# Kernel optimization log

Measured on AMD Instinct MI355X. Metric: run time of the kernel, lower is better.

## Reference

```python
import jax, jax.numpy as jnp
import numpy as np

D_MODEL = 1024
N_HEADS = 16
D_FF = 4096
DEPTH = D_MODEL // N_HEADS
EPS = 1e-5


def setup_inputs() -> dict:
    key = jax.random.key(0)
    ks = jax.random.split(key, 16)
    s = 0.02
    inp = {
        'x': jax.random.normal(ks[0], (4, 2048, D_MODEL), jnp.float32),
        'wq': jax.random.normal(ks[1], (D_MODEL, D_MODEL), jnp.float32) * s,
        'bq': jnp.zeros((D_MODEL,), jnp.float32),
        'wk': jax.random.normal(ks[2], (D_MODEL, D_MODEL), jnp.float32) * s,
        'bk': jnp.zeros((D_MODEL,), jnp.float32),
        'wv': jax.random.normal(ks[3], (D_MODEL, D_MODEL), jnp.float32) * s,
        'bv': jnp.zeros((D_MODEL,), jnp.float32),
        'wo': jax.random.normal(ks[4], (D_MODEL, D_MODEL), jnp.float32) * s,
        'bo': jnp.zeros((D_MODEL,), jnp.float32),
        'w1': jax.random.normal(ks[5], (D_MODEL, D_FF), jnp.float32) * s,
        'b1': jnp.zeros((D_FF,), jnp.float32),
        'w2': jax.random.normal(ks[6], (D_FF, D_MODEL), jnp.float32) * s,
        'b2': jnp.zeros((D_MODEL,), jnp.float32),
        'g1': jnp.ones((D_MODEL,), jnp.float32),
        'be1': jnp.zeros((D_MODEL,), jnp.float32),
        'g2': jnp.ones((D_MODEL,), jnp.float32),
        'be2': jnp.zeros((D_MODEL,), jnp.float32),
    }
    return inp


def _layernorm(x, g, b):
    mu = jnp.mean(x, -1, keepdims=True)
    var = jnp.mean((x - mu) ** 2, -1, keepdims=True)
    return (x - mu) * jax.lax.rsqrt(var + EPS) * g + b


def _rope_angles(seq_len):
    # NB: original module uses raw angles (no cos/sin applied) -- replicate faithfully
    inv_freq = 1.0 / (10000.0 ** (jnp.arange(0, DEPTH, 2, dtype=jnp.float32) / DEPTH))
    freqs = jnp.arange(seq_len, dtype=jnp.float32)[:, None] * inv_freq[None, :]  # [S, DEPTH/2]
    emb = jnp.concatenate([freqs, freqs], axis=-1)  # [S, DEPTH]
    return emb[..., 0::2], emb[..., 1::2]  # 'cos', 'sin' each [S, DEPTH/2]


def _apply_rope(t, cos, sin):
    tc, ts = t[..., 0::2], t[..., 1::2]
    return jnp.concatenate([tc * cos - ts * sin, tc * sin + ts * cos], axis=-1)


def reference(x, wq, bq, wk, bk, wv, bv, wo, bo, w1, b1, w2, b2, g1, be1, g2, be2):
    B, S, D = x.shape
    H, Dh = N_HEADS, DEPTH

    def heads(t):  # [B,S,D] -> [B,H,S,Dh]
        return t.reshape(B, S, H, Dh).transpose(0, 2, 1, 3)

    q = heads(x @ wq + bq)
    k = heads(x @ wk + bk)
    v = heads(x @ wv + bv)

    cos, sin = _rope_angles(S)  # broadcast over [B,H,S,Dh/2]
    q_rot = _apply_rope(q, cos, sin)
    k_rot = _apply_rope(k, cos, sin)

    logits = jnp.einsum('bhqd,bhkd->bhqk', q_rot, k_rot) / jnp.sqrt(jnp.float32(Dh))
    attn = jax.nn.softmax(logits, axis=-1)
    ctx = jnp.einsum('bhqk,bhkd->bhqd', attn, v)  # [B,H,S,Dh]
    ctx = ctx.transpose(0, 2, 1, 3).reshape(B, S, D)
    attn_out = ctx @ wo + bo

    h = _layernorm(x + attn_out, g1, be1)
    ff = jax.nn.relu(h @ w1 + b1) @ w2 + b2
    return _layernorm(h + ff, g2, be2)
```

## Files before the change

### kernel.cpp

```cpp
#include <hip/hip_runtime.h>

typedef _Float16 f16x8 __attribute__((ext_vector_type(8)));
typedef float    f32x4 __attribute__((ext_vector_type(4)));
typedef float    f32x2 __attribute__((ext_vector_type(2)));
typedef short    bf16x8 __attribute__((ext_vector_type(8)));

__device__ __forceinline__ float b2f(ushort u){
  union { float f; unsigned int i; } v; v.i = ((unsigned int)u) << 16; return v.f;
}
__device__ __forceinline__ ushort f2b(float f){
  union { float f; unsigned int i; } v; v.f = f;
  unsigned int r = (v.i + 0x7FFFu + ((v.i >> 16) & 1u)) >> 16;
  return (ushort)r;
}
__device__ __forceinline__ ushort f2h_u(float f){
  union { _Float16 h; ushort u; } v; v.h = (_Float16)f; return v.u;
}
__device__ __forceinline__ float ldf(const void* p, size_t i, int f){
  return f ? ((const float*)p)[i] : b2f(((const ushort*)p)[i]);
}
__device__ __forceinline__ void split3(float v, ushort& a0, ushort& a1, ushort& a2){
  a0 = f2b(v);
  const float r1 = v - b2f(a0);
  a1 = f2b(r1);
  a2 = f2b(r1 - b2f(a1));
}

__global__ void detect_k(const void* __restrict__ x, int* __restrict__ flag)
{
  const int lane = threadIdx.x;
  const ushort* p = (const ushort*)x;
  int wild = 0, zeven = 0;
#pragma unroll
  for (int j = 0; j < 8; ++j) {
    const int idx = lane * 8 + j;
    const ushort u = p[idx];
    if (((u >> 7) & 0xFF) >= 0xF1) ++wild;
    if (((idx & 1) == 0) && u == 0) ++zeven;
  }
#pragma unroll
  for (int off = 1; off < 64; off <<= 1) {
    wild += __shfl_xor(wild, off);
    zeven += __shfl_xor(zeven, off);
  }
  if (lane == 0) *flag = (wild >= 4 || zeven >= 128) ? 1 : 0;
}

__global__ void wtab_k(float* __restrict__ w, int* __restrict__ zeroc,
                       unsigned* __restrict__ ovc)
{
  const int d = threadIdx.x;
  const int i = (d >> 1) & 15;
  const double F2 = pow(10000.0, -(double)i / 8.0);
  const double G2 = pow(10000.0, -(double)(2 * i + 1) / 16.0);
  w[d] = (float)((F2 + G2) * 0.125);
  if (d == 0) { *zeroc = 0; *ovc = 0u; }
}

__global__ __launch_bounds__(256) void cvt_wT_k(const void* __restrict__ W,
    const int* __restrict__ fp, _Float16* __restrict__ Wt, int K, int N)
{
  __shared__ float t[32][33];
  const int f = *fp;
  const int n0 = blockIdx.x * 32, k0 = blockIdx.y * 32;
  const int ln = threadIdx.x & 31, lr = threadIdx.x >> 5;
#pragma unroll
  for (int u = 0; u < 4; ++u) {
    const int kk = lr + u * 8;
    t[kk][ln] = ldf(W, (size_t)(k0 + kk) * N + n0 + ln, f);
  }
  __syncthreads();
#pragma unroll
  for (int u = 0; u < 4; ++u) {
    const int nn = lr + u * 8;
    Wt[(size_t)(n0 + nn) * K + k0 + ln] = (_Float16)t[ln][nn];
  }
}

__global__ __launch_bounds__(256) void cvt_w3T_k(const void* __restrict__ W,
    const int* __restrict__ fp, ushort* __restrict__ Wt3)
{
  __shared__ float t[32][33];
  const int f = *fp;
  const int n0 = blockIdx.x * 32, k0 = blockIdx.y * 32;
  const int ln = threadIdx.x & 31, lr = threadIdx.x >> 5;
#pragma unroll
  for (int u = 0; u < 4; ++u) {
    const int kk = lr + u * 8;
    t[kk][ln] = ldf(W, (size_t)(k0 + kk) * 1024 + n0 + ln, f);
  }
  __syncthreads();
#pragma unroll
  for (int u = 0; u < 4; ++u) {
    const int nn = lr + u * 8;
    const float v = t[ln][nn];
    ushort p0, p1, p2;
    split3(v, p0, p1, p2);
    const size_t o = (size_t)(n0 + nn) * 1024 + k0 + ln;
    Wt3[o]           = p0;
    Wt3[1048576 + o] = p1;
    Wt3[2097152 + o] = p2;
  }
}

__global__ __launch_bounds__(256) void sgemm_qk(
    const void* __restrict__ A, const int* __restrict__ afp,
    const ushort* __restrict__ W3q, const ushort* __restrict__ W3k,
    const void* __restrict__ bq, const void* __restrict__ bk,
    const int* __restrict__ wfp,
    float* __restrict__ qb, float* __restrict__ kbuf,
    const float* __restrict__ wtab)
{
  __shared__ ushort As3[3][128][32];
  const int tid = threadIdx.x;
  const int lane = tid & 63, w = tid >> 6;
  const int wm = w >> 1, wn = w & 1;
  const int fr = lane & 15, g = lane >> 4;
  const int bn = blockIdx.x * 128;
  const int bm = blockIdx.y * 128;
  const int isK = bn >> 10;
  const ushort* W3 = isK ? W3k : W3q;
  const int bnl = bn & 1023;
  const int af = *afp;

  f32x4 acc[4][4];
#pragma unroll
  for (int m = 0; m < 4; ++m)
#pragma unroll
    for (int n = 0; n < 4; ++n)
      acc[m][n][0] = acc[m][n][1] = acc[m][n][2] = acc[m][n][3] = 0.f;

  for (int k0 = 0; k0 < 1024; k0 += 32) {
    __syncthreads();
    {
      const int row = tid >> 1, kk0 = (tid & 1) * 16;
      float tv[16];
      if (af) {
        const float4* p = (const float4*)((const float*)A + (size_t)(bm + row) * 1024 + k0 + kk0);
#pragma unroll
        for (int u = 0; u < 4; ++u) {
          const float4 t = p[u];
          tv[u*4]=t.x; tv[u*4+1]=t.y; tv[u*4+2]=t.z; tv[u*4+3]=t.w;
        }
      } else {
        const uint4* p = (const uint4*)((const ushort*)A + (size_t)(bm + row) * 1024 + k0 + kk0);
#pragma unroll
        for (int u = 0; u < 2; ++u) {
          const uint4 t = p[u];
          tv[u*8+0]=b2f((ushort)(t.x&0xffff)); tv[u*8+1]=b2f((ushort)(t.x>>16));
          tv[u*8+2]=b2f((ushort)(t.y&0xffff)); tv[u*8+3]=b2f((ushort)(t.y>>16));
          tv[u*8+4]=b2f((ushort)(t.z&0xffff)); tv[u*8+5]=b2f((ushort)(t.z>>16));
          tv[u*8+6]=b2f((ushort)(t.w&0xffff)); tv[u*8+7]=b2f((ushort)(t.w>>16));
        }
      }
      ushort p0[16], p1[16], p2[16];
#pragma unroll
      for (int u = 0; u < 16; ++u) split3(tv[u], p0[u], p1[u], p2[u]);
#pragma unroll
      for (int u = 0; u < 2; ++u) {
        *(uint4*)&As3[0][row][kk0 + u*8] = *(uint4*)&p0[u*8];
        *(uint4*)&As3[1][row][kk0 + u*8] = *(uint4*)&p1[u*8];
        *(uint4*)&As3[2][row][kk0 + u*8] = *(uint4*)&p2[u*8];
      }
    }
    __syncthreads();

    bf16x8 afr[3][4];
#pragma unroll
    for (int p = 0; p < 3; ++p)
#pragma unroll
      for (int m = 0; m < 4; ++m)
        afr[p][m] = *(const bf16x8*)&As3[p][wm*64 + m*16 + fr][g*8];

#pragma unroll
    for (int pb = 0; pb < 3; ++pb) {
      bf16x8 bfr[4];
#pragma unroll
      for (int n = 0; n < 4; ++n)
        bfr[n] = *(const bf16x8*)(W3 + (size_t)pb * 1048576 +
                                  (size_t)(bnl + wn*64 + n*16 + fr) * 1024 + k0 + g*8);
      const int npa = 3 - pb;
#pragma unroll
      for (int m = 0; m < 4; ++m)
#pragma unroll
        for (int n = 0; n < 4; ++n)
#pragma unroll
          for (int pa = 0; pa < 3; ++pa)
            if (pa < npa)
              acc[m][n] = __builtin_amdgcn_mfma_f32_16x16x32_bf16(
                              afr[pa][m], bfr[n], acc[m][n], 0, 0, 0);
    }
  }

  const int wf = *wfp;
#pragma unroll
  for (int m = 0; m < 4; ++m) {
#pragma unroll
    for (int n = 0; n < 4; ++n) {
      const int col = bnl + wn*64 + n*16 + fr;
      const float bv = ldf(isK ? bk : bq, col, wf);
      const int hh = col >> 6, dh = col & 63;
#pragma unroll
      for (int e = 0; e < 4; ++e) {
        const int gr = bm + wm*64 + m*16 + g*4 + e;
        const int b = gr >> 11, s = gr & 2047;
        const size_t idx = (size_t)b * 2097152 + (((size_t)hh * 2048) + s) * 64 + dh;
        const float v = acc[m][n][e] + bv;
        if (isK) kbuf[idx] = v;
        else     qb[idx]   = v * wtab[dh];
      }
    }
  }
}

__global__ __launch_bounds__(256) void vgemm_k(
    const void* __restrict__ A, const int* __restrict__ afp,
    const _Float16* __restrict__ Wt,
    const void* __restrict__ bias, const int* __restrict__ bfp,
    ushort* __restrict__ outU)
{
  __shared__ _Float16 As[128][40];
  __shared__ _Float16 Bs[128][40];
  const int tid = threadIdx.x;
  const int lane = tid & 63;
  const int w = tid >> 6;
  const int wm = w >> 1, wn = w & 1;
  const int fr = lane & 15, g = lane >> 4;
  const int bn = blockIdx.x * 128, bm = blockIdx.y * 128;
  const int af = *afp;

  f32x4 acc[4][4];
#pragma unroll
  for (int m = 0; m < 4; ++m)
#pragma unroll
    for (int n = 0; n < 4; ++n)
      acc[m][n][0] = acc[m][n][1] = acc[m][n][2] = acc[m][n][3] = 0.f;

  for (int k0 = 0; k0 < 1024; k0 += 32) {
    __syncthreads();
    {
      const int r = tid >> 1, kp = (tid & 1) * 16;
      float tv[16];
      if (af) {
        const float4* p = (const float4*)((const float*)A + (size_t)(bm + r) * 1024 + k0 + kp);
#pragma unroll
        for (int u = 0; u < 4; ++u) {
          const float4 t = p[u];
          tv[u*4]=t.x; tv[u*4+1]=t.y; tv[u*4+2]=t.z; tv[u*4+3]=t.w;
        }
      } else {
        const uint4* p = (const uint4*)((const ushort*)A + (size_t)(bm + r) * 1024 + k0 + kp);
#pragma unroll
        for (int u = 0; u < 2; ++u) {
          const uint4 t = p[u];
          tv[u*8+0]=b2f((ushort)(t.x&0xffff)); tv[u*8+1]=b2f((ushort)(t.x>>16));
          tv[u*8+2]=b2f((ushort)(t.y&0xffff)); tv[u*8+3]=b2f((ushort)(t.y>>16));
          tv[u*8+4]=b2f((ushort)(t.z&0xffff)); tv[u*8+5]=b2f((ushort)(t.z>>16));
          tv[u*8+6]=b2f((ushort)(t.w&0xffff)); tv[u*8+7]=b2f((ushort)(t.w>>16));
        }
      }
      _Float16 hv[16];
#pragma unroll
      for (int u = 0; u < 16; ++u) hv[u] = (_Float16)tv[u];
      *(uint4*)&As[r][kp]     = *(uint4*)&hv[0];
      *(uint4*)&As[r][kp + 8] = *(uint4*)&hv[8];
    }
    {
      const int r = tid >> 1, kp = (tid & 1) * 16;
      const uint4* bp = (const uint4*)(Wt + (size_t)(bn + r) * 1024 + k0 + kp);
      const uint4 v0 = bp[0], v1 = bp[1];
      *(uint4*)&Bs[r][kp]     = v0;
      *(uint4*)&Bs[r][kp + 8] = v1;
    }
    __syncthreads();
    f16x8 afr[4], bf8[4];
#pragma unroll
    for (int m = 0; m < 4; ++m)
      afr[m] = *(const f16x8*)&As[wm * 64 + m * 16 + fr][g * 8];
#pragma unroll
    for (int n = 0; n < 4; ++n)
      bf8[n] = *(const f16x8*)&Bs[wn * 64 + n * 16 + fr][g * 8];
#pragma unroll
    for (int m = 0; m < 4; ++m)
#pragma unroll
      for (int n = 0; n < 4; ++n)
        acc[m][n] = __builtin_amdgcn_mfma_f32_16x16x32_f16(afr[m], bf8[n], acc[m][n], 0, 0, 0);
  }

  const int bfl = *bfp;
#pragma unroll
  for (int m = 0; m < 4; ++m) {
#pragma unroll
    for (int n = 0; n < 4; ++n) {
      const int gc = bn + wn * 64 + n * 16 + fr;
      const float bv = ldf(bias, gc, bfl);
      const int hh = gc >> 6, dh = gc & 63;
#pragma unroll
      for (int e = 0; e < 4; ++e) {
        const int gr = bm + wm * 64 + m * 16 + g * 4 + e;
        const int b = gr >> 11, s = gr & 2047;
        const size_t idx = (size_t)b * 2097152 + (((size_t)hh * 2048) + s) * 64 + dh;
        outU[idx] = f2b(acc[m][n][e] + bv);
      }
    }
  }
}

template<int MODE>
__global__ __launch_bounds__(256) void sgemm(
    const void* __restrict__ A, const int* __restrict__ afp, int arow0,
    const void* __restrict__ W, const void* __restrict__ bias,
    const int* __restrict__ wfp,
    const void* __restrict__ res, const int* __restrict__ rfp,
    ushort* __restrict__ outU, float* __restrict__ outF,
    const float* __restrict__ wtab,
    int N, int K, int erow0)
{
  __shared__ float As[64][17];
  __shared__ float Ws[16][65];
  const int tid = threadIdx.x;
  const int tx = tid & 15, ty = tid >> 4;
  const int bn = blockIdx.x * 64, bm = blockIdx.y * 64;
  const int af = *afp, wf = *wfp;

  float acc[4][4] = {};

  for (int k0 = 0; k0 < K; k0 += 16) {
    __syncthreads();
#pragma unroll
    for (int u = 0; u < 4; ++u) {
      const int idx = tid * 4 + u;
      const int row = idx >> 4, kk = idx & 15;
      As[row][kk] = ldf(A, (size_t)(arow0 + bm + row) * K + k0 + kk, af);
    }
#pragma unroll
    for (int u = 0; u < 4; ++u) {
      const int idx = tid * 4 + u;
      const int kk = idx >> 6, col = idx & 63;
      Ws[kk][col] = ldf(W, (size_t)(k0 + kk) * N + bn + col, wf);
    }
    __syncthreads();
#pragma unroll
    for (int kk = 0; kk < 16; ++kk) {
      float ar[4], wr[4];
#pragma unroll
      for (int i = 0; i < 4; ++i) ar[i] = As[ty * 4 + i][kk];
#pragma unroll
      for (int j = 0; j < 4; ++j) wr[j] = Ws[kk][tx * 4 + j];
#pragma unroll
      for (int i = 0; i < 4; ++i)
#pragma unroll
        for (int j = 0; j < 4; ++j) acc[i][j] += ar[i] * wr[j];
    }
  }

  const int rf = (MODE >= 4) ? *rfp : 0;
#pragma unroll
  for (int i = 0; i < 4; ++i) {
    const int gr = erow0 + bm + ty * 4 + i;
#pragma unroll
    for (int j = 0; j < 4; ++j) {
      const int gc = bn + tx * 4 + j;
      float v = acc[i][j] + ldf(bias, gc, wf);
      if (MODE == 0) {
        const int hh = gc >> 6, dh = gc & 63, s = gr & 2047;
        outF[(((size_t)hh * 2048) + s) * 64 + dh] = v * wtab[dh];
      } else if (MODE == 1) {
        const int hh = gc >> 6, dh = gc & 63, s = gr & 2047;
        outF[(((size_t)hh * 2048) + s) * 64 + dh] = v;
      } else if (MODE == 2) {
        const int hh = gc >> 6, dh = gc & 63, s = gr & 2047;
        outU[(((size_t)hh * 2048) + s) * 64 + dh] = f2b(v);
      } else if (MODE == 3) {
        outU[(size_t)gr * N + gc] = f2b(fmaxf(v, 0.f));
      } else if (MODE == 4) {
        v += ldf(res, (size_t)gr * 1024 + gc, rf);
        outU[(size_t)gr * 1024 + gc] = f2b(v);
      } else {
        v += ldf(res, (size_t)gr * 1024 + gc, rf);
        outF[(size_t)gr * 1024 + gc] = v;
      }
    }
  }
}

template<int MODE, int TM>
__global__ __launch_bounds__(256) void hgemm(
    const _Float16* __restrict__ A, int arow0,
    const _Float16* __restrict__ Wt,
    const void* __restrict__ bias, const int* __restrict__ bfp,
    const void* __restrict__ res, const int* __restrict__ rfp,
    const _Float16* __restrict__ resH,
    _Float16* __restrict__ outH, float* __restrict__ outF,
    int N, int K, int erow0)
{
  constexpr int MF = TM / 32;
  __shared__ _Float16 As[TM][40];
  __shared__ _Float16 Bs[128][40];
  const int tid = threadIdx.x;
  const int lane = tid & 63;
  const int w = tid >> 6;
  const int wm = w >> 1, wn = w & 1;
  const int fr = lane & 15, g = lane >> 4;
  const int bn = blockIdx.x * 128, bm = blockIdx.y * TM;

  f32x4 acc[MF][4];
#pragma unroll
  for (int m = 0; m < MF; ++m)
#pragma unroll
    for (int n = 0; n < 4; ++n)
      acc[m][n][0] = acc[m][n][1] = acc[m][n][2] = acc[m][n][3] = 0.f;

  for (int k0 = 0; k0 < K; k0 += 32) {
    __syncthreads();
    if constexpr (TM == 128) {
      const int r = tid >> 1, kp = (tid & 1) * 16;
      const uint4* ap = (const uint4*)(A + (size_t)(arow0 + bm + r) * K + k0 + kp);
      const uint4 v0 = ap[0], v1 = ap[1];
      *(uint4*)&As[r][kp]     = v0;
      *(uint4*)&As[r][kp + 8] = v1;
    } else {
      const int r = tid >> 2, kp = (tid & 3) * 8;
      const uint4 v0 = *(const uint4*)(A + (size_t)(arow0 + bm + r) * K + k0 + kp);
      *(uint4*)&As[r][kp] = v0;
    }
    {
      const int r = tid >> 1, kp = (tid & 1) * 16;
      const uint4* bp = (const uint4*)(Wt + (size_t)(bn + r) * K + k0 + kp);
      const uint4 v0 = bp[0], v1 = bp[1];
      *(uint4*)&Bs[r][kp]     = v0;
      *(uint4*)&Bs[r][kp + 8] = v1;
    }
    __syncthreads();
    f16x8 afr[MF], bf8[4];
#pragma unroll
    for (int m = 0; m < MF; ++m)
      afr[m] = *(const f16x8*)&As[wm * (TM / 2) + m * 16 + fr][g * 8];
#pragma unroll
    for (int n = 0; n < 4; ++n)
      bf8[n] = *(const f16x8*)&Bs[wn * 64 + n * 16 + fr][g * 8];
#pragma unroll
    for (int m = 0; m < MF; ++m)
#pragma unroll
      for (int n = 0; n < 4; ++n)
        acc[m][n] = __builtin_amdgcn_mfma_f32_16x16x32_f16(afr[m], bf8[n], acc[m][n], 0, 0, 0);
  }

  const int bfl = *bfp;
  const int rfl = (MODE == 4) ? *rfp : 0;
#pragma unroll
  for (int m = 0; m < MF; ++m) {
#pragma unroll
    for (int n = 0; n < 4; ++n) {
      const int gc = bn + wn * 64 + n * 16 + fr;
      const float bv = ldf(bias, gc, bfl);
#pragma unroll
      for (int e = 0; e < 4; ++e) {
        const int gr = erow0 + bm + wm * (TM / 2) + m * 16 + (lane >> 4) * 4 + e;
        float v = acc[m][n][e] + bv;
        if (MODE == 3) {
          outH[(size_t)gr * N + gc] = (_Float16)fmaxf(v, 0.f);
        } else if (MODE == 4) {
          v += ldf(res, (size_t)gr * 1024 + gc, rfl);
          outH[(size_t)gr * 1024 + gc] = (_Float16)v;
        } else {
          v += (float)resH[(size_t)gr * 1024 + gc];
          outF[(size_t)gr * 1024 + gc] = v;
        }
      }
    }
  }
}

#define ACAP 48

__global__ __launch_bounds__(256) void attn_mfma_k(
    const float* __restrict__ qb, const float* __restrict__ kb,
    const ushort* __restrict__ vb, ushort* __restrict__ ctx,
    unsigned* __restrict__ ovcount, unsigned* __restrict__ ovlist)
{
  __shared__ __align__(16) char smem[32768];
  ushort*   kpl  = (ushort*)smem;
  unsigned* cnt  = (unsigned*)(smem + 13824);
  float*    mrow = (float*)(smem + 14080);
  ushort*   cL   = (ushort*)(smem + 14336);
  float*    LL   = (float*)(smem + 20480);

  const int tid  = threadIdx.x;
  const int lane = tid & 63;
  const int wv   = tid >> 6;
  const int fr   = lane & 15, g = lane >> 4;
  const int h = blockIdx.y, b = blockIdx.z;
  const int s0 = blockIdx.x * 64;
  const size_t bh = (size_t)b * 16 + h;
  const float*  qh = qb + bh * (2048 * 64);
  const float*  kh = kb + bh * (2048 * 64);
  const ushort* vh = vb + bh * (2048 * 64);

  {
    ushort* qs = (ushort*)smem;
    const int r = tid >> 2, d0 = (tid & 3) * 16;
    const float4* qp = (const float4*)(qh + (size_t)(s0 + r) * 64 + d0);
    float tv[16];
#pragma unroll
    for (int u = 0; u < 4; ++u) {
      const float4 t = qp[u];
      tv[u*4]=t.x; tv[u*4+1]=t.y; tv[u*4+2]=t.z; tv[u*4+3]=t.w;
    }
    ushort p0[16], p1[16], p2[16];
#pragma unroll
    for (int u = 0; u < 16; ++u) split3(tv[u], p0[u], p1[u], p2[u]);
    const int base = r * 72 + d0;
#pragma unroll
    for (int u = 0; u < 2; ++u) {
      *(uint4*)&qs[0*4608 + base + u*8] = *(uint4*)&p0[u*8];
      *(uint4*)&qs[1*4608 + base + u*8] = *(uint4*)&p1[u*8];
      *(uint4*)&qs[2*4608 + base + u*8] = *(uint4*)&p2[u*8];
    }
  }
  __syncthreads();
  bf16x8 af[3][2];
  {
    ushort* qs = (ushort*)smem;
    const int rb = (wv * 16 + fr) * 72 + g * 8;
#pragma unroll
    for (int p = 0; p < 3; ++p)
#pragma unroll
      for (int dg = 0; dg < 2; ++dg)
        af[p][dg] = *(bf16x8*)&qs[p*4608 + rb + dg*32];
  }
  __syncthreads();
  if (tid < 64) cnt[tid] = 0;

  float svv[4];
#pragma unroll
  for (int e = 0; e < 4; ++e) svv[e] = (float)(s0 + wv * 16 + g * 4 + e);

  float mloc[4] = {-3.0e38f, -3.0e38f, -3.0e38f, -3.0e38f};

  for (int c0 = 0; c0 < 2048; c0 += 32) {
    __syncthreads();
    {
      const int key = tid >> 3, d0 = (tid & 7) * 8;
      const float4* kp4 = (const float4*)(kh + (size_t)(c0 + key) * 64 + d0);
      const float4 t0 = kp4[0], t1 = kp4[1];
      float tv[8] = {t0.x,t0.y,t0.z,t0.w,t1.x,t1.y,t1.z,t1.w};
      ushort p0[8], p1[8], p2[8];
#pragma unroll
      for (int u = 0; u < 8; ++u) split3(tv[u], p0[u], p1[u], p2[u]);
      const int base = key * 72 + d0;
      *(uint4*)&kpl[0*2304 + base] = *(uint4*)&p0[0];
      *(uint4*)&kpl[1*2304 + base] = *(uint4*)&p1[0];
      *(uint4*)&kpl[2*2304 + base] = *(uint4*)&p2[0];
    }
    __syncthreads();

    float Lv[2][4];
#pragma unroll
    for (int kg = 0; kg < 2; ++kg) {
      f32x4 a0v = {0.f,0.f,0.f,0.f}, a1v = {0.f,0.f,0.f,0.f}, a2v = {0.f,0.f,0.f,0.f};
#pragma unroll
      for (int dg = 0; dg < 2; ++dg) {
        const int rb = (kg * 16 + fr) * 72 + dg * 32 + g * 8;
        const bf16x8 b0 = *(bf16x8*)&kpl[0*2304 + rb];
        const bf16x8 b1 = *(bf16x8*)&kpl[1*2304 + rb];
        const bf16x8 b2 = *(bf16x8*)&kpl[2*2304 + rb];
        a0v = __builtin_amdgcn_mfma_f32_16x16x32_bf16(af[0][dg], b0, a0v, 0,0,0);
        a1v = __builtin_amdgcn_mfma_f32_16x16x32_bf16(af[0][dg], b1, a1v, 0,0,0);
        a2v = __builtin_amdgcn_mfma_f32_16x16x32_bf16(af[1][dg], b0, a2v, 0,0,0);
        a0v = __builtin_amdgcn_mfma_f32_16x16x32_bf16(af[1][dg], b1, a0v, 0,0,0);
        a1v = __builtin_amdgcn_mfma_f32_16x16x32_bf16(af[0][dg], b2, a1v, 0,0,0);
        a2v = __builtin_amdgcn_mfma_f32_16x16x32_bf16(af[2][dg], b0, a2v, 0,0,0);
      }
      const float cw = (float)(c0 + kg * 16 + fr);
#pragma unroll
      for (int e = 0; e < 4; ++e) {
        const float a = (a0v[e] + a1v[e]) + a2v[e];
        Lv[kg][e] = a * cw * svv[e];
      }
    }
#pragma unroll
    for (int e = 0; e < 4; ++e) {
      float t = fmaxf(Lv[0][e], Lv[1][e]);
#pragma unroll
      for (int off = 1; off < 16; off <<= 1) t = fmaxf(t, __shfl_xor(t, off));
      mloc[e] = fmaxf(mloc[e], t);
    }
#pragma unroll
    for (int kg = 0; kg < 2; ++kg)
#pragma unroll
      for (int e = 0; e < 4; ++e) {
        if (Lv[kg][e] > mloc[e] - 80.f) {
          const int row = wv * 16 + g * 4 + e;
          const unsigned idx = atomicAdd(&cnt[row], 1u);
          if (idx < ACAP) {
            cL[row * ACAP + idx] = (ushort)(c0 + kg * 16 + fr);
            LL[row * ACAP + idx] = Lv[kg][e];
          }
        }
      }
  }
  if (fr == 0) {
#pragma unroll
    for (int e = 0; e < 4; ++e) mrow[wv * 16 + g * 4 + e] = mloc[e];
  }
  __syncthreads();

  const int row = tid >> 2, seg = tid & 3;
  const unsigned n = cnt[row];
  const int gs = s0 + row;
  if (n > ACAP) {
    if (seg == 0) {
      const unsigned i = atomicAdd(ovcount, 1u);
      ovlist[i] = (unsigned)(bh * 2048 + gs);
    }
  } else {
    const float mf = mrow[row];
    float o[16];
#pragma unroll
    for (int u = 0; u < 16; ++u) o[u] = 0.f;
    float l = 0.f;
    for (unsigned i = 0; i < n; ++i) {
      const float d = LL[row * ACAP + i] - mf;
      if (d > -80.f) {
        const int c = cL[row * ACAP + i];
        const float p = expf(d);
        l += p;
        const uint4* vp = (const uint4*)(vh + (size_t)c * 64 + seg * 16);
        const uint4 t0 = vp[0], t1 = vp[1];
        const uint wds[8] = {t0.x,t0.y,t0.z,t0.w,t1.x,t1.y,t1.z,t1.w};
#pragma unroll
        for (int u = 0; u < 8; ++u) {
          o[u*2]   += p * b2f((ushort)(wds[u] & 0xffff));
          o[u*2+1] += p * b2f((ushort)(wds[u] >> 16));
        }
      }
    }
    const float inv = 1.f / l;
    ushort* op = ctx + (((size_t)b * 2048) + gs) * 1024 + h * 64 + seg * 16;
    uint pk[8];
#pragma unroll
    for (int u = 0; u < 8; ++u)
      pk[u] = (uint)f2h_u(o[2*u] * inv) | ((uint)f2h_u(o[2*u+1] * inv) << 16);
    *(uint4*)(op)     = make_uint4(pk[0], pk[1], pk[2], pk[3]);
    *(uint4*)(op + 8) = make_uint4(pk[4], pk[5], pk[6], pk[7]);
  }
}

__global__ __launch_bounds__(256) void attn_cleanup2_k(
    const float* __restrict__ qb, const float* __restrict__ kb,
    const ushort* __restrict__ vb, ushort* __restrict__ ctx,
    const unsigned* __restrict__ ovcount, const unsigned* __restrict__ ovlist)
{
  __shared__ float Ls[2048];
  __shared__ float osum[32][65];
  __shared__ float wm[4], wl[4];
  const unsigned count = *ovcount;
  const int tid = threadIdx.x;
  const int seg = tid & 7;
  const int kq  = tid >> 3;
  const int wave = tid >> 6;

  for (unsigned idx = blockIdx.x; idx < count; idx += gridDim.x) {
    const unsigned r = ovlist[idx];
    const int gs = (int)(r & 2047u);
    const size_t bh = (size_t)(r >> 11);
    const int b = (int)(bh >> 4), h = (int)(bh & 15);
    const float*  qh = qb + bh * (2048 * 64);
    const float*  kh = kb + bh * (2048 * 64);
    const ushort* vh = vb + bh * (2048 * 64);

    float q[8];
    {
      const float4* qp = (const float4*)(qh + (size_t)gs * 64 + seg * 8);
      const float4 t0 = qp[0], t1 = qp[1];
      q[0]=t0.x; q[1]=t0.y; q[2]=t0.z; q[3]=t0.w;
      q[4]=t1.x; q[5]=t1.y; q[6]=t1.z; q[7]=t1.w;
    }
    const float sq = (float)gs;

    float mloc = -3.0e38f;
    for (int it = 0; it < 64; ++it) {
      const int c = it * 32 + kq;
      const float4* kp = (const float4*)(kh + (size_t)c * 64 + seg * 8);
      const float4 a = kp[0], bb = kp[1];
      float dt = q[0]*a.x + q[1]*a.y + q[2]*a.z + q[3]*a.w
               + q[4]*bb.x + q[5]*bb.y + q[6]*bb.z + q[7]*bb.w;
      dt += __shfl_xor(dt, 1);
      dt += __shfl_xor(dt, 2);
      dt += __shfl_xor(dt, 4);
      const float L = dt * sq * (float)c;
      if (seg == 0) Ls[c] = L;
      mloc = fmaxf(mloc, L);
    }
    mloc = fmaxf(mloc, __shfl_xor(mloc, 8));
    mloc = fmaxf(mloc, __shfl_xor(mloc, 16));
    mloc = fmaxf(mloc, __shfl_xor(mloc, 32));
    if ((tid & 63) == 0) wm[wave] = mloc;
    __syncthreads();
    const float m = fmaxf(fmaxf(wm[0], wm[1]), fmaxf(wm[2], wm[3]));

    float o[8] = {0.f,0.f,0.f,0.f,0.f,0.f,0.f,0.f};
    float lloc = 0.f;
    for (int it = 0; it < 64; ++it) {
      const int c = it * 32 + kq;
      const float p = expf(Ls[c] - m);
      lloc += p;
      const uint4 vv = *(const uint4*)(vh + (size_t)c * 64 + seg * 8);
      o[0] += p * b2f((ushort)(vv.x & 0xffff)); o[1] += p * b2f((ushort)(vv.x >> 16));
      o[2] += p * b2f((ushort)(vv.y & 0xffff)); o[3] += p * b2f((ushort)(vv.y >> 16));
      o[4] += p * b2f((ushort)(vv.z & 0xffff)); o[5] += p * b2f((ushort)(vv.z >> 16));
      o[6] += p * b2f((ushort)(vv.w & 0xffff)); o[7] += p * b2f((ushort)(vv.w >> 16));
    }
    lloc += __shfl_xor(lloc, 8);
    lloc += __shfl_xor(lloc, 16);
    lloc += __shfl_xor(lloc, 32);
    if ((tid & 63) == 0) wl[wave] = lloc;
#pragma unroll
    for (int u = 0; u < 8; ++u) osum[kq][seg * 8 + u] = o[u];
    __syncthreads();
    const float l = (wl[0] + wl[1]) + (wl[2] + wl[3]);
    if (tid < 64) {
      float acc = 0.f;
#pragma unroll
      for (int k2 = 0; k2 < 32; ++k2) acc += osum[k2][tid];
      ctx[(((size_t)b * 2048) + gs) * 1024 + h * 64 + tid] = f2h_u(acc / l);
    }
    __syncthreads();
  }
}

template<int RPT, int OF16>
__global__ __launch_bounds__(256) void attn_k(
    const float* __restrict__ qb, const float* __restrict__ kb,
    const ushort* __restrict__ vb, ushort* __restrict__ ctx,
    int b0, size_t bstrF, size_t bstrU)
{
  __shared__ float kS[64][64];
  __shared__ float vS[64][64];
  const int tid = threadIdx.x;
  const int h  = blockIdx.y;
  const int bz = blockIdx.z;
  const int b  = b0 + bz;
  const float*  qh = qb + bstrF * bz + (size_t)h * 2048 * 64;
  const float*  kh = kb + bstrF * bz + (size_t)h * 2048 * 64;
  const ushort* vh = vb + bstrU * bz + (size_t)h * 2048 * 64;

  const int seg  = tid & 3;
  const int slot = tid >> 2;
  const int row0 = blockIdx.x * (64 * RPT) + slot * RPT;

  f32x2 qv[RPT][8], o[RPT][8];
  float m[RPT], l[RPT], sq[RPT];
#pragma unroll
  for (int i = 0; i < RPT; ++i) {
    const float4* qp = (const float4*)(qh + (size_t)(row0 + i) * 64 + seg * 16);
#pragma unroll
    for (int w = 0; w < 4; ++w) {
      const float4 t = qp[w];
      qv[i][2*w]   = f32x2{t.x, t.y};
      qv[i][2*w+1] = f32x2{t.z, t.w};
    }
    m[i] = -3.0e38f; l[i] = 0.f; sq[i] = (float)(row0 + i);
#pragma unroll
    for (int t = 0; t < 8; ++t) o[i][t] = f32x2{0.f, 0.f};
  }

  for (int c0 = 0; c0 < 2048; c0 += 64) {
    __syncthreads();
    {
      const int key = tid >> 2, sg = tid & 3;
      const float4* sp = (const float4*)(kh + (size_t)(c0 + key) * 64 + sg * 16);
      float4* dp = (float4*)&kS[key][sg * 16];
#pragma unroll
      for (int u = 0; u < 4; ++u) dp[u] = sp[u];
      const uint4* vp = (const uint4*)(vh + (size_t)(c0 + key) * 64 + sg * 16);
      float* vd = &vS[key][sg * 16];
#pragma unroll
      for (int u = 0; u < 2; ++u) {
        const uint4 t = vp[u];
        vd[u*8+0] = b2f((ushort)(t.x & 0xffff)); vd[u*8+1] = b2f((ushort)(t.x >> 16));
        vd[u*8+2] = b2f((ushort)(t.y & 0xffff)); vd[u*8+3] = b2f((ushort)(t.y >> 16));
        vd[u*8+4] = b2f((ushort)(t.z & 0xffff)); vd[u*8+5] = b2f((ushort)(t.z >> 16));
        vd[u*8+6] = b2f((ushort)(t.w & 0xffff)); vd[u*8+7] = b2f((ushort)(t.w >> 16));
      }
    }
    __syncthreads();
#pragma unroll 2
    for (int j = 0; j < 64; ++j) {
      const float4* kp = (const float4*)&kS[j][seg * 16];
      const float4 ka = kp[0], kb4 = kp[1], kc = kp[2], kd = kp[3];
      const f32x2 K0 = {ka.x, ka.y},  K1 = {ka.z, ka.w};
      const f32x2 K2 = {kb4.x, kb4.y}, K3 = {kb4.z, kb4.w};
      const f32x2 K4 = {kc.x, kc.y},  K5 = {kc.z, kc.w};
      const f32x2 K6 = {kd.x, kd.y},  K7 = {kd.z, kd.w};
      float dt[RPT];
#pragma unroll
      for (int i = 0; i < RPT; ++i) {
        f32x2 a2 = qv[i][0] * K0;
        a2 += qv[i][1] * K1;
        a2 += qv[i][2] * K2;
        a2 += qv[i][3] * K3;
        a2 += qv[i][4] * K4;
        a2 += qv[i][5] * K5;
        a2 += qv[i][6] * K6;
        a2 += qv[i][7] * K7;
        dt[i] = a2[0] + a2[1];
      }
#pragma unroll
      for (int i = 0; i < RPT; ++i) {
        dt[i] += __shfl_xor(dt[i], 1);
        dt[i] += __shfl_xor(dt[i], 2);
      }
      const float cc = (float)(c0 + j);
#pragma unroll
      for (int i = 0; i < RPT; ++i) {
        const float L = dt[i] * sq[i] * cc;
        const float d = L - m[i];
        if (d > 0.f) {
          const float r = expf(-d);
          l[i] = l[i] * r + 1.f;
          m[i] = L;
          const f32x2 r2 = {r, r};
          const float4* vp4 = (const float4*)&vS[j][seg * 16];
          const float4 va = vp4[0], vb4 = vp4[1], vc = vp4[2], vd4 = vp4[3];
          const f32x2 V[8] = {{va.x,va.y},{va.z,va.w},{vb4.x,vb4.y},{vb4.z,vb4.w},
                              {vc.x,vc.y},{vc.z,vc.w},{vd4.x,vd4.y},{vd4.z,vd4.w}};
#pragma unroll
          for (int t = 0; t < 8; ++t) o[i][t] = o[i][t] * r2 + V[t];
        } else if (d > -80.f) {
          const float p = expf(d);
          l[i] += p;
          const f32x2 p2 = {p, p};
          const float4* vp4 = (const float4*)&vS[j][seg * 16];
          const float4 va = vp4[0], vb4 = vp4[1], vc = vp4[2], vd4 = vp4[3];
          const f32x2 V[8] = {{va.x,va.y},{va.z,va.w},{vb4.x,vb4.y},{vb4.z,vb4.w},
                              {vc.x,vc.y},{vc.z,vc.w},{vd4.x,vd4.y},{vd4.z,vd4.w}};
#pragma unroll
          for (int t = 0; t < 8; ++t) o[i][t] += p2 * V[t];
        }
      }
    }
  }

#pragma unroll
  for (int i = 0; i < RPT; ++i) {
    const float inv = 1.f / l[i];
    ushort* op = ctx + (((size_t)b * 2048) + row0 + i) * 1024 + h * 64 + seg * 16;
    uint pk[8];
#pragma unroll
    for (int t2 = 0; t2 < 8; ++t2) {
      const uint lo = OF16 ? (uint)f2h_u(o[i][t2][0] * inv) : (uint)f2b(o[i][t2][0] * inv);
      const uint hi = OF16 ? (uint)f2h_u(o[i][t2][1] * inv) : (uint)f2b(o[i][t2][1] * inv);
      pk[t2] = lo | (hi << 16);
    }
    *(uint4*)(op)     = make_uint4(pk[0], pk[1], pk[2], pk[3]);
    *(uint4*)(op + 8) = make_uint4(pk[4], pk[5], pk[6], pk[7]);
  }
}

__global__ __launch_bounds__(256) void ln_k(const ushort* __restrict__ y,
                                            const void* __restrict__ g,
                                            const void* __restrict__ be,
                                            const int* __restrict__ fp,
                                            ushort* __restrict__ out)
{
  const int row = blockIdx.x, tid = threadIdx.x;
  const int f = *fp;
  const ushort* p = y + (size_t)row * 1024;
  float v[4], s = 0.f, s2 = 0.f;
#pragma unroll
  for (int i = 0; i < 4; ++i) {
    const float x = b2f(p[tid + i * 256]);
    v[i] = x; s += x; s2 += x * x;
  }
#pragma unroll
  for (int off = 1; off < 64; off <<= 1) { s += __shfl_xor(s, off); s2 += __shfl_xor(s2, off); }
  __shared__ float red[8];
  const int wave = tid >> 6, lane = tid & 63;
  if (lane == 0) { red[wave] = s; red[4 + wave] = s2; }
  __syncthreads();
  s = red[0] + red[1] + red[2] + red[3];
  s2 = red[4] + red[5] + red[6] + red[7];
  const float mu = s * (1.f / 1024.f);
  const float var = s2 * (1.f / 1024.f) - mu * mu;
  const float rstd = rsqrtf(var + 1e-5f);
  ushort* o = out + (size_t)row * 1024;
#pragma unroll
  for (int i = 0; i < 4; ++i) {
    const int c = tid + i * 256;
    o[c] = f2b((v[i] - mu) * rstd * ldf(g, c, f) + ldf(be, c, f));
  }
}

__global__ __launch_bounds__(256) void ln_h_k(const _Float16* __restrict__ y,
                                              const void* __restrict__ g,
                                              const void* __restrict__ be,
                                              const int* __restrict__ fp,
                                              _Float16* __restrict__ out)
{
  const int row = blockIdx.x, tid = threadIdx.x;
  const int f = *fp;
  const _Float16* p = y + (size_t)row * 1024;
  float v[4], s = 0.f, s2 = 0.f;
#pragma unroll
  for (int i = 0; i < 4; ++i) {
    const float x = (float)p[tid + i * 256];
    v[i] = x; s += x; s2 += x * x;
  }
#pragma unroll
  for (int off = 1; off < 64; off <<= 1) { s += __shfl_xor(s, off); s2 += __shfl_xor(s2, off); }
  __shared__ float red[8];
  const int wave = tid >> 6, lane = tid & 63;
  if (lane == 0) { red[wave] = s; red[4 + wave] = s2; }
  __syncthreads();
  s = red[0] + red[1] + red[2] + red[3];
  s2 = red[4] + red[5] + red[6] + red[7];
  const float mu = s * (1.f / 1024.f);
  const float var = s2 * (1.f / 1024.f) - mu * mu;
  const float rstd = rsqrtf(var + 1e-5f);
  _Float16* o = out + (size_t)row * 1024;
#pragma unroll
  for (int i = 0; i < 4; ++i) {
    const int c = tid + i * 256;
    o[c] = (_Float16)((v[i] - mu) * rstd * ldf(g, c, f) + ldf(be, c, f));
  }
}

__global__ __launch_bounds__(256) void ln_f32_k(float* __restrict__ y,
                                                const void* __restrict__ g,
                                                const void* __restrict__ be,
                                                const int* __restrict__ fp)
{
  const int row = blockIdx.x, tid = threadIdx.x;
  const int f = *fp;
  float* p = y + (size_t)row * 1024;
  float v[4], s = 0.f, s2 = 0.f;
#pragma unroll
  for (int i = 0; i < 4; ++i) {
    const float x = p[tid + i * 256];
    v[i] = x; s += x; s2 += x * x;
  }
#pragma unroll
  for (int off = 1; off < 64; off <<= 1) { s += __shfl_xor(s, off); s2 += __shfl_xor(s2, off); }
  __shared__ float red[8];
  const int wave = tid >> 6, lane = tid & 63;
  if (lane == 0) { red[wave] = s; red[4 + wave] = s2; }
  __syncthreads();
  s = red[0] + red[1] + red[2] + red[3];
  s2 = red[4] + red[5] + red[6] + red[7];
  const float mu = s * (1.f / 1024.f);
  const float var = s2 * (1.f / 1024.f) - mu * mu;
  const float rstd = rsqrtf(var + 1e-5f);
#pragma unroll
  for (int i = 0; i < 4; ++i) {
    const int c = tid + i * 256;
    p[c] = (v[i] - mu) * rstd * ldf(g, c, f) + ldf(be, c, f);
  }
}

extern "C" void kernel_launch(void* const* d_in, const int* in_sizes, int n_in,
                              void* d_out, int out_size, void* d_ws, size_t ws_size,
                              hipStream_t stream)
{
  const void* x  = d_in[0];
  const void* wq = d_in[1];  const void* bq = d_in[2];
  const void* wk = d_in[3];  const void* bk = d_in[4];
  const void* wv = d_in[5];  const void* bv = d_in[6];
  const void* wo = d_in[7];  const void* bo = d_in[8];
  const void* w1 = d_in[9];  const void* b1 = d_in[10];
  const void* w2 = d_in[11]; const void* b2 = d_in[12];
  const void* g1 = d_in[13]; const void* be1 = d_in[14];
  const void* g2 = d_in[15]; const void* be2 = d_in[16];
  float* outp = (float*)d_out;

  const size_t MB = 1048576;
  char* ws = (char*)d_ws;
  int*      flag    = (int*)(ws + 0);
  int*      zeroc   = (int*)(ws + 64);
  unsigned* ovcount = (unsigned*)(ws + 128);
  float*    wtab    = (float*)(ws + 256);

  detect_k<<<dim3(1), dim3(64), 0, stream>>>(x, flag);
  wtab_k<<<dim3(1), dim3(64), 0, stream>>>(wtab, zeroc, ovcount);

  const size_t QS = (size_t)16 * 2048 * 64;

  if (ws_size >= (size_t)98 * MB) {
    float*     qb   = (float*)(ws + 1 * MB);
    float*     kb   = (float*)(ws + 33 * MB);
    ushort*    vb   = (ushort*)(ws + 65 * MB);
    ushort*    ctxh = (ushort*)(ws + 81 * MB);
    unsigned*  ovlist = (unsigned*)(ws + 97 * MB);
    ushort*    W3qT = (ushort*)(ws + 81 * MB);
    ushort*    W3kT = (ushort*)(ws + 87 * MB);
    _Float16*  WvT  = (_Float16*)(ws + 93 * MB);
    _Float16*  WoT  = (_Float16*)(ws + 65 * MB);
    _Float16*  W1T  = (_Float16*)(ws + 67 * MB);
    _Float16*  W2T  = (_Float16*)(ws + 75 * MB);
    _Float16*  y1h  = (_Float16*)(ws + 1 * MB);
    _Float16*  hh   = (_Float16*)(ws + 17 * MB);
    _Float16*  ffc  = (_Float16*)(ws + 33 * MB);

    cvt_w3T_k<<<dim3(32, 32), 256, 0, stream>>>(wq, flag, W3qT);
    cvt_w3T_k<<<dim3(32, 32), 256, 0, stream>>>(wk, flag, W3kT);
    cvt_wT_k<<<dim3(32, 32),  256, 0, stream>>>(wv, flag, WvT, 1024, 1024);

    sgemm_qk<<<dim3(16, 64), 256, 0, stream>>>(x, flag, W3qT, W3kT,
                                               bq, bk, flag, qb, kb, wtab);
    vgemm_k<<<dim3(8, 64), 256, 0, stream>>>(x, flag, WvT, bv, flag, vb);

    attn_mfma_k<<<dim3(32, 16, 4), 256, 0, stream>>>(qb, kb, vb, ctxh,
                                                     ovcount, ovlist);
    attn_cleanup2_k<<<dim3(8192), 256, 0, stream>>>(qb, kb, vb, ctxh,
                                                    ovcount, ovlist);

    cvt_wT_k<<<dim3(32, 32),  256, 0, stream>>>(wo, flag, WoT, 1024, 1024);
    cvt_wT_k<<<dim3(128, 32), 256, 0, stream>>>(w1, flag, W1T, 1024, 4096);

    hgemm<4, 128><<<dim3(8, 64), 256, 0, stream>>>((const _Float16*)ctxh, 0, WoT,
                                                   bo, flag, x, flag, nullptr,
                                                   y1h, nullptr, 1024, 1024, 0);
    cvt_wT_k<<<dim3(32, 128), 256, 0, stream>>>(w2, flag, W2T, 4096, 1024);

    ln_h_k<<<dim3(8192), 256, 0, stream>>>(y1h, g1, be1, flag, hh);

    for (int c = 0; c < 2; ++c) {
      hgemm<3, 128><<<dim3(32, 32), 256, 0, stream>>>(hh, c * 4096, W1T,
                                                      b1, flag, nullptr, zeroc, nullptr,
                                                      ffc, nullptr, 4096, 1024, 0);
      hgemm<5, 64><<<dim3(8, 64), 256, 0, stream>>>(ffc, 0, W2T,
                                                    b2, flag, nullptr, zeroc, hh,
                                                    nullptr, outp, 1024, 4096, c * 4096);
    }
    ln_f32_k<<<dim3(8192), 256, 0, stream>>>(outp, g2, be2, flag);
  } else {
    float*  qb   = (float*)(ws + 1 * MB);
    float*  kb   = (float*)(ws + 9 * MB);
    ushort* vb   = (ushort*)(ws + 17 * MB);
    ushort* ctxb = (ushort*)(ws + 22 * MB);
    ushort* y1   = (ushort*)(ws + 1 * MB);
    ushort* hbuf = (ushort*)(ws + 22 * MB);
    ushort* ffc  = (ushort*)(ws + 1 * MB);

    for (int b = 0; b < 4; ++b) {
      sgemm<0><<<dim3(16, 32), 256, 0, stream>>>(x, flag, b * 2048, wq, bq, flag,
                                                 nullptr, nullptr, nullptr, qb, wtab,
                                                 1024, 1024, b * 2048);
      sgemm<1><<<dim3(16, 32), 256, 0, stream>>>(x, flag, b * 2048, wk, bk, flag,
                                                 nullptr, nullptr, nullptr, kb, wtab,
                                                 1024, 1024, b * 2048);
      sgemm<2><<<dim3(16, 32), 256, 0, stream>>>(x, flag, b * 2048, wv, bv, flag,
                                                 nullptr, nullptr, vb, nullptr, wtab,
                                                 1024, 1024, b * 2048);
      attn_k<1, 0><<<dim3(32, 16, 1), 256, 0, stream>>>(qb, kb, vb, ctxb, b, 0, 0);
    }

    sgemm<4><<<dim3(16, 128), 256, 0, stream>>>(ctxb, zeroc, 0, wo, bo, flag,
                                                x, flag, y1, nullptr, wtab,
                                                1024, 1024, 0);
    ln_k<<<dim3(8192), 256, 0, stream>>>(y1, g1, be1, flag, hbuf);
    for (int c = 0; c < 4; ++c) {
      sgemm<3><<<dim3(64, 32), 256, 0, stream>>>(hbuf, zeroc, c * 2048, w1, b1, flag,
                                                 nullptr, nullptr, ffc, nullptr, wtab,
                                                 4096, 1024, 0);
      sgemm<5><<<dim3(16, 32), 256, 0, stream>>>(ffc, zeroc, 0, w2, b2, flag,
                                                 hbuf, zeroc, nullptr, outp, wtab,
                                                 1024, 4096, c * 2048);
    }
    ln_f32_k<<<dim3(8192), 256, 0, stream>>>(outp, g2, be2, flag);
  }
}
```

Measured before the change: 1.238 ms.

## Rewrite fp16 GEMM to read B fragments from global and unchunk the FFN

```diff
diff --git a/kernel.cpp b/kernel.cpp
--- a/kernel.cpp
+++ b/kernel.cpp
@@ -384,8 +384,8 @@
   }
 }
 
-template<int MODE, int TM>
-__global__ __launch_bounds__(256) void hgemm(
+template<int MODE>
+__global__ __launch_bounds__(256) void hgemm2(
     const _Float16* __restrict__ A, int arow0,
     const _Float16* __restrict__ Wt,
     const void* __restrict__ bias, const int* __restrict__ bfp,
@@ -394,69 +394,62 @@
     _Float16* __restrict__ outH, float* __restrict__ outF,
     int N, int K, int erow0)
 {
-  constexpr int MF = TM / 32;
-  __shared__ _Float16 As[TM][40];
-  __shared__ _Float16 Bs[128][40];
+  __shared__ _Float16 As[128][72];
   const int tid = threadIdx.x;
   const int lane = tid & 63;
   const int w = tid >> 6;
   const int wm = w >> 1, wn = w & 1;
   const int fr = lane & 15, g = lane >> 4;
-  const int bn = blockIdx.x * 128, bm = blockIdx.y * TM;
-
-  f32x4 acc[MF][4];
-#pragma unroll
-  for (int m = 0; m < MF; ++m)
+  const int bn = blockIdx.x * 128, bm = blockIdx.y * 128;
+
+  f32x4 acc[4][4];
+#pragma unroll
+  for (int m = 0; m < 4; ++m)
 #pragma unroll
     for (int n = 0; n < 4; ++n)
       acc[m][n][0] = acc[m][n][1] = acc[m][n][2] = acc[m][n][3] = 0.f;
 
-  for (int k0 = 0; k0 < K; k0 += 32) {
-    __syncthreads();
-    if constexpr (TM == 128) {
-      const int r = tid >> 1, kp = (tid & 1) * 16;
+  for (int k0 = 0; k0 < K; k0 += 64) {
+    __syncthreads();
+    {
+      const int r = tid >> 1, kp = (tid & 1) * 32;
       const uint4* ap = (const uint4*)(A + (size_t)(arow0 + bm + r) * K + k0 + kp);
-      const uint4 v0 = ap[0], v1 = ap[1];
-      *(uint4*)&As[r][kp]     = v0;
-      *(uint4*)&As[r][kp + 8] = v1;
-    } else {
-      const int r = tid >> 2, kp = (tid & 3) * 8;
-      const uint4 v0 = *(const uint4*)(A + (size_t)(arow0 + bm + r) * K + k0 + kp);
-      *(uint4*)&As[r][kp] = v0;
-    }
-    {
-      const int r = tid >> 1, kp = (tid & 1) * 16;
-      const uint4* bp = (const uint4*)(Wt + (size_t)(bn + r) * K + k0 + kp);
-      const uint4 v0 = bp[0], v1 = bp[1];
-      *(uint4*)&Bs[r][kp]     = v0;
-      *(uint4*)&Bs[r][kp + 8] = v1;
-    }
-    __syncthreads();
-    f16x8 afr[MF], bf8[4];
-#pragma unroll
-    for (int m = 0; m < MF; ++m)
-      afr[m] = *(const f16x8*)&As[wm * (TM / 2) + m * 16 + fr][g * 8];
-#pragma unroll
-    for (int n = 0; n < 4; ++n)
-      bf8[n] = *(const f16x8*)&Bs[wn * 64 + n * 16 + fr][g * 8];
-#pragma unroll
-    for (int m = 0; m < MF; ++m)
+      const uint4 v0 = ap[0], v1 = ap[1], v2 = ap[2], v3 = ap[3];
+      *(uint4*)&As[r][kp]      = v0;
+      *(uint4*)&As[r][kp + 8]  = v1;
+      *(uint4*)&As[r][kp + 16] = v2;
+      *(uint4*)&As[r][kp + 24] = v3;
+    }
+    __syncthreads();
+#pragma unroll
+    for (int kh = 0; kh < 2; ++kh) {
+      f16x8 afr[4], bfr[4];
+#pragma unroll
+      for (int m = 0; m < 4; ++m)
+        afr[m] = *(const f16x8*)&As[wm * 64 + m * 16 + fr][kh * 32 + g * 8];
 #pragma unroll
       for (int n = 0; n < 4; ++n)
-        acc[m][n] = __builtin_amdgcn_mfma_f32_16x16x32_f16(afr[m], bf8[n], acc[m][n], 0, 0, 0);
+        bfr[n] = *(const f16x8*)(Wt + (size_t)(bn + wn * 64 + n * 16 + fr) * K
+                                 + k0 + kh * 32 + g * 8);
+#pragma unroll
+      for (int m = 0; m < 4; ++m)
+#pragma unroll
+        for (int n = 0; n < 4; ++n)
+          acc[m][n] = __builtin_amdgcn_mfma_f32_16x16x32_f16(afr[m], bfr[n], acc[m][n], 0, 0, 0);
+    }
   }
 
   const int bfl = *bfp;
   const int rfl = (MODE == 4) ? *rfp : 0;
 #pragma unroll
-  for (int m = 0; m < MF; ++m) {
+  for (int m = 0; m < 4; ++m) {
 #pragma unroll
     for (int n = 0; n < 4; ++n) {
       const int gc = bn + wn * 64 + n * 16 + fr;
       const float bv = ldf(bias, gc, bfl);
 #pragma unroll
       for (int e = 0; e < 4; ++e) {
-        const int gr = erow0 + bm + wm * (TM / 2) + m * 16 + (lane >> 4) * 4 + e;
+        const int gr = erow0 + bm + wm * 64 + m * 16 + g * 4 + e;
         float v = acc[m][n][e] + bv;
         if (MODE == 3) {
           outH[(size_t)gr * N + gc] = (_Float16)fmaxf(v, 0.f);
@@ -996,10 +989,10 @@
     ushort*    W3kT = (ushort*)(ws + 87 * MB);
     _Float16*  WvT  = (_Float16*)(ws + 93 * MB);
     _Float16*  WoT  = (_Float16*)(ws + 65 * MB);
-    _Float16*  W1T  = (_Float16*)(ws + 67 * MB);
-    _Float16*  W2T  = (_Float16*)(ws + 75 * MB);
     _Float16*  y1h  = (_Float16*)(ws + 1 * MB);
     _Float16*  hh   = (_Float16*)(ws + 17 * MB);
+    _Float16*  W1T  = (_Float16*)(ws + 1 * MB);
+    _Float16*  W2T  = (_Float16*)(ws + 9 * MB);
     _Float16*  ffc  = (_Float16*)(ws + 33 * MB);
 
     cvt_w3T_k<<<dim3(32, 32), 256, 0, stream>>>(wq, flag, W3qT);
@@ -1015,24 +1008,20 @@
     attn_cleanup2_k<<<dim3(8192), 256, 0, stream>>>(qb, kb, vb, ctxh,
                                                     ovcount, ovlist);
 
-    cvt_wT_k<<<dim3(32, 32),  256, 0, stream>>>(wo, flag, WoT, 1024, 1024);
+    cvt_wT_k<<<dim3(32, 32), 256, 0, stream>>>(wo, flag, WoT, 1024, 1024);
+    hgemm2<4><<<dim3(8, 64), 256, 0, stream>>>((const _Float16*)ctxh, 0, WoT,
+                                               bo, flag, x, flag, nullptr,
+                                               y1h, nullptr, 1024, 1024, 0);
+    ln_h_k<<<dim3(8192), 256, 0, stream>>>(y1h, g1, be1, flag, hh);
+
     cvt_wT_k<<<dim3(128, 32), 256, 0, stream>>>(w1, flag, W1T, 1024, 4096);
-
-    hgemm<4, 128><<<dim3(8, 64), 256, 0, stream>>>((const _Float16*)ctxh, 0, WoT,
-                                                   bo, flag, x, flag, nullptr,
-                                                   y1h, nullptr, 1024, 1024, 0);
     cvt_wT_k<<<dim3(32, 128), 256, 0, stream>>>(w2, flag, W2T, 4096, 1024);
-
-    ln_h_k<<<dim3(8192), 256, 0, stream>>>(y1h, g1, be1, flag, hh);
-
-    for (int c = 0; c < 2; ++c) {
-      hgemm<3, 128><<<dim3(32, 32), 256, 0, stream>>>(hh, c * 4096, W1T,
-                                                      b1, flag, nullptr, zeroc, nullptr,
-                                                      ffc, nullptr, 4096, 1024, 0);
-      hgemm<5, 64><<<dim3(8, 64), 256, 0, stream>>>(ffc, 0, W2T,
-                                                    b2, flag, nullptr, zeroc, hh,
-                                                    nullptr, outp, 1024, 4096, c * 4096);
-    }
+    hgemm2<3><<<dim3(32, 64), 256, 0, stream>>>(hh, 0, W1T,
+                                                b1, flag, nullptr, zeroc, nullptr,
+                                                ffc, nullptr, 4096, 1024, 0);
+    hgemm2<5><<<dim3(8, 64), 256, 0, stream>>>(ffc, 0, W2T,
+                                               b2, flag, nullptr, zeroc, hh,
+                                               nullptr, outp, 1024, 4096, 0);
     ln_f32_k<<<dim3(8192), 256, 0, stream>>>(outp, g2, be2, flag);
   } else {
     float*  qb   = (float*)(ws + 1 * MB);
```

Result: slower. 1.296 ms (+4.7%).
